# Kernel tuning notes

Hardware: AMD Instinct MI355X
Metric: run time of the kernel (lower is better)

Reference implementation:

```python
import jax, jax.numpy as jnp
import numpy as np

D_MODEL = 256      # cfg.d_model
D_INPUT = 64       # cfg.d_input == n_bands
MEM = 10           # cfg.memory_length
NSYNC = 32         # cfg.n_synch_out
ITERS = 2          # cfg.iterations (internal CTM ticks per audio frame)
VOCAB = 15
MINW = 16          # SynapseUNET minimum width; depth=2 -> widths [256, 16]
MHD = 2            # memory_hidden_dims
SYNC_DIM = NSYNC * (NSYNC + 1) // 2  # 528 upper-tri pairwise products


def _ln(x, g, b, eps=1e-5):
    m = x.mean(-1, keepdims=True)
    v = ((x - m) ** 2).mean(-1, keepdims=True)
    return (x - m) * jax.lax.rsqrt(v + eps) * g + b


def _glu(x):
    a, b = jnp.split(x, 2, axis=-1)
    return a * jax.nn.sigmoid(b)


def setup_inputs() -> dict:
    key = jax.random.key(0)
    ks = iter(jax.random.split(key, 40))
    def rn(shape, fan_in):
        return jax.random.uniform(next(ks), shape, jnp.float32, -1.0, 1.0) / np.sqrt(fan_in)
    B, T = 16, 1500
    z = jnp.zeros
    o = jnp.ones
    return {
        "batch_features": jax.random.normal(next(ks), (B, T, D_INPUT), jnp.float32),
        # learned initial traces
        "start_trace": rn((D_MODEL, MEM), MEM),
        "start_activated_trace": rn((D_MODEL, MEM), MEM),
        # classic-control backbone: Linear(64->64) + ReLU
        "Wb": rn((D_INPUT, D_INPUT), D_INPUT), "bb": z((D_INPUT,)),
        # SynapseUNET depth=2, widths [256,16]; input dim = d_input + d_model = 320
        "Wf": rn((D_INPUT + D_MODEL, 2 * D_MODEL), D_INPUT + D_MODEL), "bf": z((2 * D_MODEL,)),
        "gf": o((D_MODEL,)), "bef": z((D_MODEL,)),
        "Wd": rn((D_MODEL, 2 * MINW), D_MODEL), "bd": z((2 * MINW,)),
        "gd": o((MINW,)), "bed": z((MINW,)),
        "Wu": rn((MINW, 2 * D_MODEL), MINW), "bu": z((2 * D_MODEL,)),
        "gu": o((D_MODEL,)), "beu": z((D_MODEL,)),
        "gs": o((D_MODEL,)), "bes": z((D_MODEL,)),
        # deep neuron-level models (per-neuron MLP over the memory trace)
        "w1": rn((MEM, D_MODEL, 2 * MHD), MEM), "b1": z((1, D_MODEL, 2 * MHD)),
        "w2": rn((MHD, D_MODEL, 2), MHD), "b2": z((1, D_MODEL, 2)),
        # output head Linear(528 -> 15)
        "Wh": rn((SYNC_DIM, VOCAB), SYNC_DIM), "bh": z((VOCAB,)),
    }


def reference(batch_features, start_trace, start_activated_trace, Wb, bb,
              Wf, bf, gf, bef, Wd, bd, gd, bed, Wu, bu, gu, beu, gs, bes,
              w1, b1, w2, b2, Wh, bh):
    B = batch_features.shape[0]
    iu, ju = np.triu_indices(NSYNC)  # static index pattern (528 pairs)

    st0 = jnp.broadcast_to(start_trace, (B, D_MODEL, MEM))
    ast0 = jnp.broadcast_to(start_activated_trace, (B, D_MODEL, MEM))

    def synapses(x):  # (B, 320) -> (B, 256), U-Net with one down/up level
        h0 = _ln(_glu(x @ Wf + bf), gf, bef)        # (B, 256)
        d1 = _ln(_glu(h0 @ Wd + bd), gd, bed)       # (B, 16)
        u0 = _ln(_glu(d1 @ Wu + bu), gu, beu)       # (B, 256)
        return _ln(u0 + h0, gs, bes)                # skip + LN

    def nlm(trace):  # per-neuron MLP over memory: (B, 256, 10) -> (B, 256)
        h = _glu(jnp.einsum('bdm,mdh->bdh', trace, w1) + b1)  # (B, 256, 2)
        h = _glu(jnp.einsum('bdm,mdh->bdh', h, w2) + b2)      # (B, 256, 1)
        return h[..., 0]

    def step(carry, x_t):
        st, ast = carry
        kv = jax.nn.relu(x_t @ Wb + bb)  # backbone features (B, 64)
        act = ast[:, :, -1]
        for _ in range(ITERS):  # internal CTM ticks (fixed, small)
            pre = jnp.concatenate([kv, act], axis=-1)             # (B, 320)
            state = synapses(pre)                                  # (B, 256)
            st = jnp.concatenate([st[:, :, 1:], state[:, :, None]], axis=-1)
            act = nlm(st)                                          # (B, 256)
            ast = jnp.concatenate([ast[:, :, 1:], act[:, :, None]], axis=-1)
        sel = act[:, :NSYNC]  # 'first-last': out-sync uses first n_synch_out neurons
        sync = (sel[:, :, None] * sel[:, None, :])[:, iu, ju]      # (B, 528)
        return (st, ast), sync @ Wh + bh                            # (B, 15)

    _, logits = jax.lax.scan(step, (st0, ast0), jnp.swapaxes(batch_features, 0, 1))
    return jnp.swapaxes(logits, 0, 1)  # (B, T, vocab)
```

## Files before the change

### kernel.cpp

```cpp
#include <hip/hip_runtime.h>
#include <math.h>

#define T_LEN 1500
#define DM 256
#define DI 64
#define MEMN 10
#define SYNCD 528
#define VOC 15

typedef _Float16 f16x2 __attribute__((ext_vector_type(2)));
typedef _Float16 f16x8 __attribute__((ext_vector_type(8)));

#define FDOT2(a, b, c) __builtin_amdgcn_fdot2((a), (b), (c), false)

static __device__ __forceinline__ float dot8(f16x8 w, f16x8 q, float acc) {
  acc = FDOT2(__builtin_shufflevector(w, w, 0, 1), __builtin_shufflevector(q, q, 0, 1), acc);
  acc = FDOT2(__builtin_shufflevector(w, w, 2, 3), __builtin_shufflevector(q, q, 2, 3), acc);
  acc = FDOT2(__builtin_shufflevector(w, w, 4, 5), __builtin_shufflevector(q, q, 4, 5), acc);
  acc = FDOT2(__builtin_shufflevector(w, w, 6, 7), __builtin_shufflevector(q, q, 6, 7), acc);
  return acc;
}
static __device__ __forceinline__ f16x2 pack2(float a, float b) {
  f16x2 r; r.x = (_Float16)a; r.y = (_Float16)b; return r;
}
static __device__ __forceinline__ float sigm(float x) { return 1.0f / (1.0f + __expf(-x)); }

#define DPP_TERM(x, ctrl, rmask) \
  __int_as_float(__builtin_amdgcn_update_dpp(0, __float_as_int(x), (ctrl), (rmask), 0xF, true))
#define DPPADD(x, ctrl, rmask) (x) += DPP_TERM(x, ctrl, rmask)
#define WSUM2(a, b) do { \
  DPPADD(a, 0x111, 0xF); DPPADD(b, 0x111, 0xF); \
  DPPADD(a, 0x112, 0xF); DPPADD(b, 0x112, 0xF); \
  DPPADD(a, 0x114, 0xF); DPPADD(b, 0x114, 0xF); \
  DPPADD(a, 0x118, 0xF); DPPADD(b, 0x118, 0xF); \
  DPPADD(a, 0x142, 0xA); DPPADD(b, 0x142, 0xA); \
  DPPADD(a, 0x143, 0xC); DPPADD(b, 0x143, 0xC); \
} while (0)
static __device__ __forceinline__ float readlane_f(float x, int l) {
  return __int_as_float(__builtin_amdgcn_readlane(__float_as_int(x), l));
}

struct Params {
  const float *x, *st0, *ast0, *Wb, *bb, *Wf, *bf, *gf, *bef,
              *Wd, *bd, *gd, *bed, *Wu, *bu, *gu, *beu, *gs, *bes,
              *w1, *b1, *w2, *b2, *Wh, *bh;
  float* out;
};

struct Smem {
  float4 W1v[MEMN * DM];
  float4 W2v[DM];
  float4 B1v[DM];
  float2 B2v[DM];
  float Bf[2 * DM];
  float Bu[2 * DM];
  float Bd[32];
  float Gf[DM], Bef[DM], Gu[DM], Beu[DM], Gs[DM], Bes[DM];
  float Gd[16], Bed[16];
  float Bh[16];
  float Bb[DI];
  __attribute__((aligned(16))) float St[MEMN * DM];
  __attribute__((aligned(16))) float H0[DM];
  float Act[DM];
  __attribute__((aligned(16))) float D1[16];
  float X2[2][DI];
  __attribute__((aligned(16))) f16x2 Pre2[160];
  float PartD[16 * 33];
  float PartK[512];
  float PartH[240];
  float2 RedAB[8];
  float2 Red2AB[8];
  float Prod[SYNCD];
  float WhL[SYNCD * VOC];
  int Pair[SYNCD];
};

#define FOR20(X) X(0) X(1) X(2) X(3) X(4) X(5) X(6) X(7) X(8) X(9) \
                 X(10) X(11) X(12) X(13) X(14) X(15) X(16) X(17) X(18) X(19)

#define DECLW(i) f16x8 wa##i, wb##i;
#define LOADW(i) { const float* Wc = P.Wf + (size_t)(p160 + (i) * 8) * 512 + ch; \
  f16x8 ta, tb; \
  _Pragma("unroll") for (int e = 0; e < 8; ++e) { \
    ta[e] = (_Float16)Wc[e * 512]; tb[e] = (_Float16)Wc[e * 512 + 256]; } \
  wa##i = ta; wb##i = tb; }
#define DOT0(i) { f16x8 q = pr8[i]; aA0 = dot8(wa##i, q, aA0); aB0 = dot8(wb##i, q, aB0); }
#define DOT1(i) { f16x8 q = pr8[i]; aA1 = dot8(wa##i, q, aA1); aB1 = dot8(wb##i, q, aB1); }
#define DOTSEQ DOT0(0) DOT1(1) DOT0(2) DOT1(3) DOT0(4) DOT1(5) DOT0(6) DOT1(7) DOT0(8) DOT1(9) \
               DOT0(10) DOT1(11) DOT0(12) DOT1(13) DOT0(14) DOT1(15) DOT0(16) DOT1(17) DOT0(18) DOT1(19)

__global__ __launch_bounds__(512) __attribute__((amdgpu_waves_per_eu(2, 2)))
void ctm_kernel(Params P) {
  const int tid = threadIdx.x;
  const int b = blockIdx.x;
  __shared__ Smem sm_s;
  Smem* sm = &sm_s;

  for (int i = tid; i < MEMN * DM; i += 512) sm->W1v[i] = ((const float4*)P.w1)[i];
  if (tid < DM) {
    float2 a = ((const float2*)P.w2)[tid];
    float2 c = ((const float2*)P.w2)[DM + tid];
    float4 w; w.x = a.x; w.y = a.y; w.z = c.x; w.w = c.y;
    sm->W2v[tid] = w;
    sm->B1v[tid] = ((const float4*)P.b1)[tid];
    sm->B2v[tid] = ((const float2*)P.b2)[tid];
    sm->Gf[tid] = P.gf[tid]; sm->Bef[tid] = P.bef[tid];
    sm->Gu[tid] = P.gu[tid]; sm->Beu[tid] = P.beu[tid];
    sm->Gs[tid] = P.gs[tid]; sm->Bes[tid] = P.bes[tid];
  }
  sm->Bf[tid] = P.bf[tid];
  sm->Bu[tid] = P.bu[tid];
  if (tid < 32) sm->Bd[tid] = P.bd[tid];
  if (tid < 16) { sm->Gd[tid] = P.gd[tid]; sm->Bed[tid] = P.bed[tid]; }
  if (tid < VOC) sm->Bh[tid] = P.bh[tid];
  if (tid < DI) sm->Bb[tid] = P.bb[tid];
  for (int i = tid; i < MEMN * DM; i += 512) {
    int m = i >> 8, d = i & 255;
    sm->St[m * DM + d] = P.st0[d * MEMN + m];
  }
  if (tid < DI) sm->X2[0][tid] = P.x[(size_t)b * T_LEN * DI + tid];
  for (int i = tid; i < SYNCD * VOC; i += 512) sm->WhL[i] = P.Wh[i];
  for (int pp = tid; pp < SYNCD; pp += 512) {
    int i = 0, cum = 0;
    while (pp >= cum + (32 - i)) { cum += 32 - i; ++i; }
    sm->Pair[pp] = (i << 8) | (i + (pp - cum));
  }

  const int p = tid & 1;
  const int ch = tid >> 1;
  const int p160 = p * 160;
  FOR20(DECLW)
  FOR20(LOADW)
  const int jD = tid & 31, kcD = tid >> 5;
  float wd[16];
  #pragma unroll
  for (int q = 0; q < 16; ++q) wd[q] = P.Wd[(kcD * 16 + q) * 32 + jD];
  float wua[8], wub[8];
  #pragma unroll
  for (int q = 0; q < 8; ++q) {
    wua[q] = P.Wu[(p * 8 + q) * 512 + ch];
    wub[q] = P.Wu[(p * 8 + q) * 512 + ch + 256];
  }
  const int jK = tid & 63, kcK = tid >> 6;
  float wbr[8];
  #pragma unroll
  for (int q = 0; q < 8; ++q) wbr[q] = P.Wb[(kcK * 8 + q) * 64 + jK];

  __syncthreads();

  {
    float s = 0.f;
    #pragma unroll
    for (int q = 0; q < 8; ++q) s += sm->X2[0][kcK * 8 + q] * wbr[q];
    sm->PartK[kcK * 64 + jK] = s;
    if ((tid & 3) == 0) {
      int e = tid >> 2;
      float a0 = P.ast0[(2 * e) * MEMN + (MEMN - 1)];
      float a1 = P.ast0[(2 * e + 1) * MEMN + (MEMN - 1)];
      sm->Pre2[32 + e] = pack2(a0, a1);
    }
  }
  __syncthreads();
  if (tid >= 256 && tid < 320) {
    int j = tid - 256;
    float kv = sm->Bb[j];
    #pragma unroll
    for (int kc = 0; kc < 8; ++kc) kv += sm->PartK[kc * 64 + j];
    kv = fmaxf(kv, 0.f);
    float kn = DPP_TERM(kv, 0xB1, 0xF);
    if ((j & 1) == 0) sm->Pre2[j >> 1] = pack2(kv, kn);
  }
  __syncthreads();

  int head = 0;
  for (int t = 0; t < T_LEN; ++t) {
    float xr = 0.f;
    if (tid < DI && t + 1 < T_LEN) xr = P.x[((size_t)b * T_LEN + (t + 1)) * DI + tid];

    for (int it = 0; it < 2; ++it) {
      if (it == 1 && tid < DI) sm->X2[(t + 1) & 1][tid] = xr;
      float aA0 = 0.f, aA1 = 0.f, aB0 = 0.f, aB1 = 0.f;
      const f16x8* pr8 = (const f16x8*)(sm->Pre2 + p * 80);
      DOTSEQ
      float av = aA0 + aA1, bv = aB0 + aB1;
      DPPADD(av, 0xB1, 0xF);
      DPPADD(bv, 0xB1, 0xF);
      av += sm->Bf[ch]; bv += sm->Bf[DM + ch];
      float g = av * sigm(bv);
      float s1 = g, s2 = g * g;
      WSUM2(s1, s2);
      if ((tid & 63) == 63) { float2 r; r.x = s1; r.y = s2; sm->RedAB[tid >> 6] = r; }
      __syncthreads();

      float S1 = 0.f, S2 = 0.f;
      #pragma unroll
      for (int w = 0; w < 8; ++w) { float2 r = sm->RedAB[w]; S1 += r.x; S2 += r.y; }
      float mean = S1 * (1.0f / 512.0f);
      float var = S2 * (1.0f / 512.0f) - mean * mean;
      float h0v = (g - mean) * rsqrtf(var + 1e-5f) * sm->Gf[ch] + sm->Bef[ch];
      if (!p) sm->H0[ch] = h0v;
      __syncthreads();

      {
        float s = 0.f;
        #pragma unroll
        for (int qq = 0; qq < 4; ++qq) {
          float4 hv = ((const float4*)sm->H0)[kcD * 4 + qq];
          s += hv.x * wd[qq * 4 + 0] + hv.y * wd[qq * 4 + 1]
             + hv.z * wd[qq * 4 + 2] + hv.w * wd[qq * 4 + 3];
        }
        sm->PartD[kcD * 33 + jD] = s;
      }
      __syncthreads();

      if (tid < 32) {
        int j = tid & 15;
        float s = 0.f;
        #pragma unroll
        for (int kc = 0; kc < 16; ++kc) s += sm->PartD[kc * 33 + (tid >> 4) * 16 + j];
        float oth = __shfl_xor(s, 16);
        float gg = (s + sm->Bd[j]) * sigm(oth + sm->Bd[16 + j]);
        float t1 = gg, t2 = gg * gg;
        DPPADD(t1, 0x111, 0xF); DPPADD(t2, 0x111, 0xF);
        DPPADD(t1, 0x112, 0xF); DPPADD(t2, 0x112, 0xF);
        DPPADD(t1, 0x114, 0xF); DPPADD(t2, 0x114, 0xF);
        DPPADD(t1, 0x118, 0xF); DPPADD(t2, 0x118, 0xF);
        float T1 = readlane_f(t1, 15), T2 = readlane_f(t2, 15);
        float mn = T1 * (1.0f / 16.0f), vr = T2 * (1.0f / 16.0f) - mn * mn;
        float d1 = (gg - mn) * rsqrtf(vr + 1e-5f) * sm->Gd[j] + sm->Bed[j];
        if (tid < 16) sm->D1[j] = d1;
      }
      __syncthreads();

      float gu;
      {
        const float4* d4 = (const float4*)sm->D1;
        float4 dl = d4[p * 2], dh = d4[p * 2 + 1];
        float ua = dl.x * wua[0] + dl.y * wua[1] + dl.z * wua[2] + dl.w * wua[3]
                 + dh.x * wua[4] + dh.y * wua[5] + dh.z * wua[6] + dh.w * wua[7];
        float ub = dl.x * wub[0] + dl.y * wub[1] + dl.z * wub[2] + dl.w * wub[3]
                 + dh.x * wub[4] + dh.y * wub[5] + dh.z * wub[6] + dh.w * wub[7];
        DPPADD(ua, 0xB1, 0xF);
        DPPADD(ub, 0xB1, 0xF);
        ua += sm->Bu[ch]; ub += sm->Bu[DM + ch];
        gu = ua * sigm(ub);
        float t1 = gu, t2 = gu * gu;
        WSUM2(t1, t2);
        if ((tid & 63) == 63) { float2 r; r.x = t1; r.y = t2; sm->RedAB[tid >> 6] = r; }
      }
      __syncthreads();

      float x2v;
      {
        float U1 = 0.f, U2 = 0.f;
        #pragma unroll
        for (int w = 0; w < 8; ++w) { float2 r = sm->RedAB[w]; U1 += r.x; U2 += r.y; }
        float mn = U1 * (1.0f / 512.0f), vr = U2 * (1.0f / 512.0f) - mn * mn;
        float u0 = (gu - mn) * rsqrtf(vr + 1e-5f) * sm->Gu[ch] + sm->Beu[ch];
        x2v = u0 + h0v;
        float t1 = x2v, t2 = x2v * x2v;
        WSUM2(t1, t2);
        if ((tid & 63) == 63) { float2 r; r.x = t1; r.y = t2; sm->Red2AB[tid >> 6] = r; }
      }
      __syncthreads();

      {
        float V1 = 0.f, V2 = 0.f;
        #pragma unroll
        for (int w = 0; w < 8; ++w) { float2 r = sm->Red2AB[w]; V1 += r.x; V2 += r.y; }
        float mn = V1 * (1.0f / 512.0f), vr = V2 * (1.0f / 512.0f) - mn * mn;
        float state = (x2v - mn) * rsqrtf(vr + 1e-5f) * sm->Gs[ch] + sm->Bes[ch];
        if (!p) sm->St[head * DM + ch] = state;
        float4 h1 = sm->B1v[ch];
        int base = head + 1; if (base >= MEMN) base -= MEMN;
        #pragma unroll
        for (int m = 0; m < MEMN - 1; ++m) {
          int slot = base + m; if (slot >= MEMN) slot -= MEMN;
          float tr = sm->St[slot * DM + ch];
          float4 wv = sm->W1v[m * DM + ch];
          h1.x += tr * wv.x; h1.y += tr * wv.y; h1.z += tr * wv.z; h1.w += tr * wv.w;
        }
        {
          float4 wv = sm->W1v[(MEMN - 1) * DM + ch];
          h1.x += state * wv.x; h1.y += state * wv.y; h1.z += state * wv.z; h1.w += state * wv.w;
        }
        float g0 = h1.x * sigm(h1.z), g1 = h1.y * sigm(h1.w);
        float4 w2v = sm->W2v[ch];
        float2 b2v = sm->B2v[ch];
        float o0 = g0 * w2v.x + g1 * w2v.z + b2v.x;
        float o1 = g0 * w2v.y + g1 * w2v.w + b2v.y;
        float act = o0 * sigm(o1);
        if (!p) sm->Act[ch] = act;
        float an = DPP_TERM(act, 0x4E, 0xF);
        if ((tid & 3) == 0) sm->Pre2[32 + (tid >> 2)] = pack2(act, an);
        head += 1; if (head >= MEMN) head = 0;
      }
      __syncthreads();
    }

    {
      int pr = sm->Pair[tid];
      sm->Prod[tid] = sm->Act[pr >> 8] * sm->Act[pr & 255];
      if (tid < SYNCD - 512) {
        int pr2 = sm->Pair[512 + tid];
        sm->Prod[512 + tid] = sm->Act[pr2 >> 8] * sm->Act[pr2 & 255];
      }
      const float* X = sm->X2[(t + 1) & 1];
      float s = 0.f;
      #pragma unroll
      for (int q = 0; q < 8; ++q) s += X[kcK * 8 + q] * wbr[q];
      sm->PartK[kcK * 64 + jK] = s;
      if (t > 0 && tid < VOC) {
        float o = sm->Bh[tid];
        #pragma unroll
        for (int kc2 = 0; kc2 < 16; ++kc2) o += sm->PartH[kc2 * 15 + tid];
        P.out[((size_t)b * T_LEN + (t - 1)) * VOC + tid] = o;
      }
    }
    __syncthreads();

    if (tid < 240) {
      int kc = (tid * 4370) >> 16;
      int v = tid - kc * 15;
      float s = 0.f;
      #pragma unroll
      for (int q = 0; q < 33; ++q) {
        int pp = kc * 33 + q;
        s += sm->Prod[pp] * sm->WhL[pp * 15 + v];
      }
      sm->PartH[kc * 15 + v] = s;
    } else if (tid >= 256 && tid < 320) {
      int j = tid - 256;
      float kv = sm->Bb[j];
      #pragma unroll
      for (int kc = 0; kc < 8; ++kc) kv += sm->PartK[kc * 64 + j];
      kv = fmaxf(kv, 0.f);
      float kn = DPP_TERM(kv, 0xB1, 0xF);
      if ((j & 1) == 0) sm->Pre2[j >> 1] = pack2(kv, kn);
    }
    __syncthreads();
  }

  if (tid < VOC) {
    float o = sm->Bh[tid];
    #pragma unroll
    for (int kc = 0; kc < 16; ++kc) o += sm->PartH[kc * 15 + tid];
    P.out[((size_t)b * T_LEN + (T_LEN - 1)) * VOC + tid] = o;
  }
}

extern "C" void kernel_launch(void* const* d_in, const int* in_sizes, int n_in,
                              void* d_out, int out_size, void* d_ws, size_t ws_size,
                              hipStream_t stream) {
  (void)d_ws; (void)ws_size; (void)n_in; (void)out_size;
  Params P;
  P.x   = (const float*)d_in[0];
  P.st0 = (const float*)d_in[1];
  P.ast0= (const float*)d_in[2];
  P.Wb  = (const float*)d_in[3];
  P.bb  = (const float*)d_in[4];
  P.Wf  = (const float*)d_in[5];
  P.bf  = (const float*)d_in[6];
  P.gf  = (const float*)d_in[7];
  P.bef = (const float*)d_in[8];
  P.Wd  = (const float*)d_in[9];
  P.bd  = (const float*)d_in[10];
  P.gd  = (const float*)d_in[11];
  P.bed = (const float*)d_in[12];
  P.Wu  = (const float*)d_in[13];
  P.bu  = (const float*)d_in[14];
  P.gu  = (const float*)d_in[15];
  P.beu = (const float*)d_in[16];
  P.gs  = (const float*)d_in[17];
  P.bes = (const float*)d_in[18];
  P.w1  = (const float*)d_in[19];
  P.b1  = (const float*)d_in[20];
  P.w2  = (const float*)d_in[21];
  P.b2  = (const float*)d_in[22];
  P.Wh  = (const float*)d_in[23];
  P.bh  = (const float*)d_in[24];
  P.out = (float*)d_out;

  int B = in_sizes[0] / (T_LEN * DI);
  hipLaunchKernelGGL(ctm_kernel, dim3(B), dim3(512), 0, stream, P);
}
```

Baseline: 12.81 ms.

## Fuse two layernorm reductions into one by algebraic expansion of second-norm statistics

The second layernorm's sum and sum-of-squares are expanded algebraically in terms of moments of the GLU output, gamma and the residual term. All nine moments are reduced in one wave/block pass, which removes a full block barrier and reduction round from each of the two internal ticks. The sums of Gu and Gu squared are precomputed once before the time loop. This adds more DPP reduction work per round and may lose precision through cancellation in the expanded variance.

```diff
diff --git a/kernel.cpp b/kernel.cpp
--- a/kernel.cpp
+++ b/kernel.cpp
@@ -35,6 +35,11 @@
   DPPADD(a, 0x118, 0xF); DPPADD(b, 0x118, 0xF); \
   DPPADD(a, 0x142, 0xA); DPPADD(b, 0x142, 0xA); \
   DPPADD(a, 0x143, 0xC); DPPADD(b, 0x143, 0xC); \
+} while (0)
+#define ST9(ctrl, rm) do { \
+  DPPADD(v0, ctrl, rm); DPPADD(v1, ctrl, rm); DPPADD(v2, ctrl, rm); \
+  DPPADD(v3, ctrl, rm); DPPADD(v4, ctrl, rm); DPPADD(v5, ctrl, rm); \
+  DPPADD(v6, ctrl, rm); DPPADD(v7, ctrl, rm); DPPADD(v8, ctrl, rm); \
 } while (0)
 static __device__ __forceinline__ float readlane_f(float x, int l) {
   return __int_as_float(__builtin_amdgcn_readlane(__float_as_int(x), l));
@@ -69,7 +74,8 @@
   float PartK[512];
   float PartH[240];
   float2 RedAB[8];
-  float2 Red2AB[8];
+  __attribute__((aligned(16))) float RedW[8][12];
+  float SGc[4];
   float Prod[SYNCD];
   float WhL[SYNCD * VOC];
   int Pair[SYNCD];
@@ -159,8 +165,18 @@
       float a1 = P.ast0[(2 * e + 1) * MEMN + (MEMN - 1)];
       sm->Pre2[32 + e] = pack2(a0, a1);
     }
+    float gv = sm->Gu[ch];
+    float gv2 = gv * gv;
+    WSUM2(gv, gv2);
+    if ((tid & 63) == 63) { float2 r; r.x = gv; r.y = gv2; sm->RedAB[tid >> 6] = r; }
   }
   __syncthreads();
+  if (tid == 0) {
+    float sg = 0.f, sg2 = 0.f;
+    #pragma unroll
+    for (int w = 0; w < 8; ++w) { float2 r = sm->RedAB[w]; sg += r.x; sg2 += r.y; }
+    sm->SGc[0] = sg; sm->SGc[1] = sg2;
+  }
   if (tid >= 256 && tid < 320) {
     int j = tid - 256;
     float kv = sm->Bb[j];
@@ -232,7 +248,7 @@
       }
       __syncthreads();
 
-      float gu;
+      float gu, Gch, Cch;
       {
         const float4* d4 = (const float4*)sm->D1;
         float4 dl = d4[p * 2], dh = d4[p * 2 + 1];
@@ -244,40 +260,63 @@
         DPPADD(ub, 0xB1, 0xF);
         ua += sm->Bu[ch]; ub += sm->Bu[DM + ch];
         gu = ua * sigm(ub);
-        float t1 = gu, t2 = gu * gu;
-        WSUM2(t1, t2);
-        if ((tid & 63) == 63) { float2 r; r.x = t1; r.y = t2; sm->RedAB[tid >> 6] = r; }
-      }
-      __syncthreads();
-
-      float x2v;
+        Gch = sm->Gu[ch];
+        Cch = sm->Beu[ch] + h0v;
+        float A = gu * Gch;
+        float v0 = gu, v1 = gu * gu, v2 = A, v3 = A * A, v4 = A * Cch,
+              v5 = A * Gch, v6 = Cch, v7 = Cch * Cch, v8 = Gch * Cch;
+        ST9(0x111, 0xF);
+        ST9(0x112, 0xF);
+        ST9(0x114, 0xF);
+        ST9(0x118, 0xF);
+        ST9(0x142, 0xA);
+        ST9(0x143, 0xC);
+        if ((tid & 63) == 63) {
+          float4* rw = (float4*)sm->RedW[tid >> 6];
+          float4 q0; q0.x = v0; q0.y = v1; q0.z = v2; q0.w = v3;
+          float4 q1; q1.x = v4; q1.y = v5; q1.z = v6; q1.w = v7;
+          float4 q2; q2.x = v8; q2.y = 0.f; q2.z = 0.f; q2.w = 0.f;
+          rw[0] = q0; rw[1] = q1; rw[2] = q2;
+        }
+      }
+      __syncthreads();
+
       {
-        float U1 = 0.f, U2 = 0.f;
+        float4 a0; a0.x = 0.f; a0.y = 0.f; a0.z = 0.f; a0.w = 0.f;
+        float4 a1 = a0, a2 = a0;
         #pragma unroll
-        for (int w = 0; w < 8; ++w) { float2 r = sm->RedAB[w]; U1 += r.x; U2 += r.y; }
-        float mn = U1 * (1.0f / 512.0f), vr = U2 * (1.0f / 512.0f) - mn * mn;
-        float u0 = (gu - mn) * rsqrtf(vr + 1e-5f) * sm->Gu[ch] + sm->Beu[ch];
-        x2v = u0 + h0v;
-        float t1 = x2v, t2 = x2v * x2v;
-        WSUM2(t1, t2);
-        if ((tid & 63) == 63) { float2 r; r.x = t1; r.y = t2; sm->Red2AB[tid >> 6] = r; }
-      }
-      __syncthreads();
-
-      {
-        float V1 = 0.f, V2 = 0.f;
-        #pragma unroll
-        for (int w = 0; w < 8; ++w) { float2 r = sm->Red2AB[w]; V1 += r.x; V2 += r.y; }
-        float mn = V1 * (1.0f / 512.0f), vr = V2 * (1.0f / 512.0f) - mn * mn;
-        float state = (x2v - mn) * rsqrtf(vr + 1e-5f) * sm->Gs[ch] + sm->Bes[ch];
+        for (int w = 0; w < 8; ++w) {
+          const float4* rw = (const float4*)sm->RedW[w];
+          float4 q0 = rw[0], q1 = rw[1], q2 = rw[2];
+          a0.x += q0.x; a0.y += q0.y; a0.z += q0.z; a0.w += q0.w;
+          a1.x += q1.x; a1.y += q1.y; a1.z += q1.z; a1.w += q1.w;
+          a2.x += q2.x;
+        }
+        float Sgu = a0.x, Sgu2 = a0.y, SA = a0.z, SA2 = a0.w;
+        float SAC = a1.x, SAG = a1.y, SC = a1.z, SC2 = a1.w;
+        float SGC = a2.x;
+        float SG = sm->SGc[0], SG2 = sm->SGc[1];
+        float m = Sgu * (1.0f / 512.0f);
+        float vr_ = Sgu2 * (1.0f / 512.0f) - m * m;
+        float r = rsqrtf(vr_ + 1e-5f);
+        float u0 = (gu - m) * r * Gch + (Cch - h0v);
+        float x2v = u0 + h0v;
+        float rm = r * m;
+        float S1x = r * SA - rm * SG + SC;
+        float S2x = r * r * SA2 + SC2 + rm * rm * SG2
+                  + 2.0f * r * SAC - 2.0f * r * rm * SAG - 2.0f * rm * SGC;
+        float mx = S1x * (1.0f / 512.0f);
+        float varx = S2x * (1.0f / 512.0f) - mx * mx;
+        float rx = rsqrtf(varx + 1e-5f);
+        float state = (x2v - mx) * rx * sm->Gs[ch] + sm->Bes[ch];
         if (!p) sm->St[head * DM + ch] = state;
         float4 h1 = sm->B1v[ch];
         int base = head + 1; if (base >= MEMN) base -= MEMN;
         #pragma unroll
-        for (int m = 0; m < MEMN - 1; ++m) {
-          int slot = base + m; if (slot >= MEMN) slot -= MEMN;
+        for (int mm = 0; mm < MEMN - 1; ++mm) {
+          int slot = base + mm; if (slot >= MEMN) slot -= MEMN;
           float tr = sm->St[slot * DM + ch];
-          float4 wv = sm->W1v[m * DM + ch];
+          float4 wv = sm->W1v[mm * DM + ch];
           h1.x += tr * wv.x; h1.y += tr * wv.y; h1.z += tr * wv.z; h1.w += tr * wv.w;
         }
         {
```

Result: slower. 18.50 ms (+44.4%).

## Pack two batch elements per 1024-thread block sharing weight tables

Applied to the files above, without the earlier changes.

Each workgroup now processes two batch elements with 1024 threads, sharing the LDS weight tables while giving each element its own private state buffers. With B=16 this halves the grid to 8 blocks. The intent is presumably to cut the redundant per-block weight staging and share one CU's LDS. The cost is that both elements run on one CU and sync at every barrier, and waves_per_eu rises to 4, which halves the per-thread register budget even though each thread still holds 40 f16x8 weight registers, so spilling is likely.

```diff
diff --git a/kernel.cpp b/kernel.cpp
--- a/kernel.cpp
+++ b/kernel.cpp
@@ -47,6 +47,21 @@
   float* out;
 };
 
+struct SmemEl {
+  __attribute__((aligned(16))) float St[MEMN * DM];
+  __attribute__((aligned(16))) float H0[DM];
+  float Act[DM];
+  __attribute__((aligned(16))) float D1[16];
+  float X2[2][DI];
+  __attribute__((aligned(16))) f16x2 Pre2[160];
+  float PartD[16 * 33];
+  float PartK[512];
+  float PartH[240];
+  float2 RedAB[8];
+  float2 Red2AB[8];
+  float Prod[SYNCD];
+};
+
 struct Smem {
   float4 W1v[MEMN * DM];
   float4 W2v[DM];
@@ -59,20 +74,9 @@
   float Gd[16], Bed[16];
   float Bh[16];
   float Bb[DI];
-  __attribute__((aligned(16))) float St[MEMN * DM];
-  __attribute__((aligned(16))) float H0[DM];
-  float Act[DM];
-  __attribute__((aligned(16))) float D1[16];
-  float X2[2][DI];
-  __attribute__((aligned(16))) f16x2 Pre2[160];
-  float PartD[16 * 33];
-  float PartK[512];
-  float PartH[240];
-  float2 RedAB[8];
-  float2 Red2AB[8];
-  float Prod[SYNCD];
   float WhL[SYNCD * VOC];
   int Pair[SYNCD];
+  SmemEl el[2];
 };
 
 #define FOR20(X) X(0) X(1) X(2) X(3) X(4) X(5) X(6) X(7) X(8) X(9) \
@@ -89,14 +93,17 @@
 #define DOTSEQ DOT0(0) DOT1(1) DOT0(2) DOT1(3) DOT0(4) DOT1(5) DOT0(6) DOT1(7) DOT0(8) DOT1(9) \
                DOT0(10) DOT1(11) DOT0(12) DOT1(13) DOT0(14) DOT1(15) DOT0(16) DOT1(17) DOT0(18) DOT1(19)
 
-__global__ __launch_bounds__(512) __attribute__((amdgpu_waves_per_eu(2, 2)))
+__global__ __launch_bounds__(1024) __attribute__((amdgpu_waves_per_eu(4, 4)))
 void ctm_kernel(Params P) {
   const int tid = threadIdx.x;
-  const int b = blockIdx.x;
+  const int elid = tid >> 9;
+  const int ltid = tid & 511;
+  const int b = blockIdx.x * 2 + elid;
   __shared__ Smem sm_s;
   Smem* sm = &sm_s;
-
-  for (int i = tid; i < MEMN * DM; i += 512) sm->W1v[i] = ((const float4*)P.w1)[i];
+  SmemEl* E = &sm_s.el[elid];
+
+  for (int i = tid; i < MEMN * DM; i += 1024) sm->W1v[i] = ((const float4*)P.w1)[i];
   if (tid < DM) {
     float2 a = ((const float2*)P.w2)[tid];
     float2 c = ((const float2*)P.w2)[DM + tid];
@@ -108,30 +115,30 @@
     sm->Gu[tid] = P.gu[tid]; sm->Beu[tid] = P.beu[tid];
     sm->Gs[tid] = P.gs[tid]; sm->Bes[tid] = P.bes[tid];
   }
-  sm->Bf[tid] = P.bf[tid];
-  sm->Bu[tid] = P.bu[tid];
+  if (tid < 2 * DM) { sm->Bf[tid] = P.bf[tid]; sm->Bu[tid] = P.bu[tid]; }
   if (tid < 32) sm->Bd[tid] = P.bd[tid];
   if (tid < 16) { sm->Gd[tid] = P.gd[tid]; sm->Bed[tid] = P.bed[tid]; }
   if (tid < VOC) sm->Bh[tid] = P.bh[tid];
   if (tid < DI) sm->Bb[tid] = P.bb[tid];
-  for (int i = tid; i < MEMN * DM; i += 512) {
-    int m = i >> 8, d = i & 255;
-    sm->St[m * DM + d] = P.st0[d * MEMN + m];
-  }
-  if (tid < DI) sm->X2[0][tid] = P.x[(size_t)b * T_LEN * DI + tid];
-  for (int i = tid; i < SYNCD * VOC; i += 512) sm->WhL[i] = P.Wh[i];
-  for (int pp = tid; pp < SYNCD; pp += 512) {
+  for (int i = tid; i < SYNCD * VOC; i += 1024) sm->WhL[i] = P.Wh[i];
+  for (int pp = tid; pp < SYNCD; pp += 1024) {
     int i = 0, cum = 0;
     while (pp >= cum + (32 - i)) { cum += 32 - i; ++i; }
     sm->Pair[pp] = (i << 8) | (i + (pp - cum));
   }
 
-  const int p = tid & 1;
-  const int ch = tid >> 1;
+  for (int i = ltid; i < MEMN * DM; i += 512) {
+    int m = i >> 8, d = i & 255;
+    E->St[m * DM + d] = P.st0[d * MEMN + m];
+  }
+  if (ltid < DI) E->X2[0][ltid] = P.x[(size_t)b * T_LEN * DI + ltid];
+
+  const int p = ltid & 1;
+  const int ch = ltid >> 1;
   const int p160 = p * 160;
   FOR20(DECLW)
   FOR20(LOADW)
-  const int jD = tid & 31, kcD = tid >> 5;
+  const int jD = ltid & 31, kcD = ltid >> 5;
   float wd[16];
   #pragma unroll
   for (int q = 0; q < 16; ++q) wd[q] = P.Wd[(kcD * 16 + q) * 32 + jD];
@@ -141,7 +148,7 @@
     wua[q] = P.Wu[(p * 8 + q) * 512 + ch];
     wub[q] = P.Wu[(p * 8 + q) * 512 + ch + 256];
   }
-  const int jK = tid & 63, kcK = tid >> 6;
+  const int jK = ltid & 63, kcK = ltid >> 6;
   float wbr[8];
   #pragma unroll
   for (int q = 0; q < 8; ++q) wbr[q] = P.Wb[(kcK * 8 + q) * 64 + jK];
@@ -151,36 +158,36 @@
   {
     float s = 0.f;
     #pragma unroll
-    for (int q = 0; q < 8; ++q) s += sm->X2[0][kcK * 8 + q] * wbr[q];
-    sm->PartK[kcK * 64 + jK] = s;
-    if ((tid & 3) == 0) {
-      int e = tid >> 2;
+    for (int q = 0; q < 8; ++q) s += E->X2[0][kcK * 8 + q] * wbr[q];
+    E->PartK[kcK * 64 + jK] = s;
+    if ((ltid & 3) == 0) {
+      int e = ltid >> 2;
       float a0 = P.ast0[(2 * e) * MEMN + (MEMN - 1)];
       float a1 = P.ast0[(2 * e + 1) * MEMN + (MEMN - 1)];
-      sm->Pre2[32 + e] = pack2(a0, a1);
+      E->Pre2[32 + e] = pack2(a0, a1);
     }
   }
   __syncthreads();
-  if (tid >= 256 && tid < 320) {
-    int j = tid - 256;
+  if (ltid >= 256 && ltid < 320) {
+    int j = ltid - 256;
     float kv = sm->Bb[j];
     #pragma unroll
-    for (int kc = 0; kc < 8; ++kc) kv += sm->PartK[kc * 64 + j];
+    for (int kc = 0; kc < 8; ++kc) kv += E->PartK[kc * 64 + j];
     kv = fmaxf(kv, 0.f);
     float kn = DPP_TERM(kv, 0xB1, 0xF);
-    if ((j & 1) == 0) sm->Pre2[j >> 1] = pack2(kv, kn);
+    if ((j & 1) == 0) E->Pre2[j >> 1] = pack2(kv, kn);
   }
   __syncthreads();
 
   int head = 0;
   for (int t = 0; t < T_LEN; ++t) {
     float xr = 0.f;
-    if (tid < DI && t + 1 < T_LEN) xr = P.x[((size_t)b * T_LEN + (t + 1)) * DI + tid];
+    if (ltid < DI && t + 1 < T_LEN) xr = P.x[((size_t)b * T_LEN + (t + 1)) * DI + ltid];
 
     for (int it = 0; it < 2; ++it) {
-      if (it == 1 && tid < DI) sm->X2[(t + 1) & 1][tid] = xr;
+      if (it == 1 && ltid < DI) E->X2[(t + 1) & 1][ltid] = xr;
       float aA0 = 0.f, aA1 = 0.f, aB0 = 0.f, aB1 = 0.f;
-      const f16x8* pr8 = (const f16x8*)(sm->Pre2 + p * 80);
+      const f16x8* pr8 = (const f16x8*)(E->Pre2 + p * 80);
       DOTSEQ
       float av = aA0 + aA1, bv = aB0 + aB1;
       DPPADD(av, 0xB1, 0xF);
@@ -189,35 +196,35 @@
       float g = av * sigm(bv);
       float s1 = g, s2 = g * g;
       WSUM2(s1, s2);
-      if ((tid & 63) == 63) { float2 r; r.x = s1; r.y = s2; sm->RedAB[tid >> 6] = r; }
+      if ((ltid & 63) == 63) { float2 r; r.x = s1; r.y = s2; E->RedAB[ltid >> 6] = r; }
       __syncthreads();
 
       float S1 = 0.f, S2 = 0.f;
       #pragma unroll
-      for (int w = 0; w < 8; ++w) { float2 r = sm->RedAB[w]; S1 += r.x; S2 += r.y; }
+      for (int w = 0; w < 8; ++w) { float2 r = E->RedAB[w]; S1 += r.x; S2 += r.y; }
       float mean = S1 * (1.0f / 512.0f);
       float var = S2 * (1.0f / 512.0f) - mean * mean;
       float h0v = (g - mean) * rsqrtf(var + 1e-5f) * sm->Gf[ch] + sm->Bef[ch];
-      if (!p) sm->H0[ch] = h0v;
+      if (!p) E->H0[ch] = h0v;
       __syncthreads();
 
       {
         float s = 0.f;
         #pragma unroll
         for (int qq = 0; qq < 4; ++qq) {
-          float4 hv = ((const float4*)sm->H0)[kcD * 4 + qq];
+          float4 hv = ((const float4*)E->H0)[kcD * 4 + qq];
           s += hv.x * wd[qq * 4 + 0] + hv.y * wd[qq * 4 + 1]
              + hv.z * wd[qq * 4 + 2] + hv.w * wd[qq * 4 + 3];
         }
-        sm->PartD[kcD * 33 + jD] = s;
-      }
-      __syncthreads();
-
-      if (tid < 32) {
-        int j = tid & 15;
+        E->PartD[kcD * 33 + jD] = s;
+      }
+      __syncthreads();
+
+      if (ltid < 32) {
+        int j = ltid & 15;
         float s = 0.f;
         #pragma unroll
-        for (int kc = 0; kc < 16; ++kc) s += sm->PartD[kc * 33 + (tid >> 4) * 16 + j];
+        for (int kc = 0; kc < 16; ++kc) s += E->PartD[kc * 33 + (ltid >> 4) * 16 + j];
         float oth = __shfl_xor(s, 16);
         float gg = (s + sm->Bd[j]) * sigm(oth + sm->Bd[16 + j]);
         float t1 = gg, t2 = gg * gg;
@@ -228,13 +235,13 @@
         float T1 = readlane_f(t1, 15), T2 = readlane_f(t2, 15);
         float mn = T1 * (1.0f / 16.0f), vr = T2 * (1.0f / 16.0f) - mn * mn;
         float d1 = (gg - mn) * rsqrtf(vr + 1e-5f) * sm->Gd[j] + sm->Bed[j];
-        if (tid < 16) sm->D1[j] = d1;
+        if (ltid < 16) E->D1[j] = d1;
       }
       __syncthreads();
 
       float gu;
       {
-        const float4* d4 = (const float4*)sm->D1;
+        const float4* d4 = (const float4*)E->D1;
         float4 dl = d4[p * 2], dh = d4[p * 2 + 1];
         float ua = dl.x * wua[0] + dl.y * wua[1] + dl.z * wua[2] + dl.w * wua[3]
                  + dh.x * wua[4] + dh.y * wua[5] + dh.z * wua[6] + dh.w * wua[7];
@@ -246,7 +253,7 @@
         gu = ua * sigm(ub);
         float t1 = gu, t2 = gu * gu;
         WSUM2(t1, t2);
-        if ((tid & 63) == 63) { float2 r; r.x = t1; r.y = t2; sm->RedAB[tid >> 6] = r; }
+        if ((ltid & 63) == 63) { float2 r; r.x = t1; r.y = t2; E->RedAB[ltid >> 6] = r; }
       }
       __syncthreads();
 
@@ -254,29 +261,29 @@
       {
         float U1 = 0.f, U2 = 0.f;
         #pragma unroll
-        for (int w = 0; w < 8; ++w) { float2 r = sm->RedAB[w]; U1 += r.x; U2 += r.y; }
+        for (int w = 0; w < 8; ++w) { float2 r = E->RedAB[w]; U1 += r.x; U2 += r.y; }
         float mn = U1 * (1.0f / 512.0f), vr = U2 * (1.0f / 512.0f) - mn * mn;
         float u0 = (gu - mn) * rsqrtf(vr + 1e-5f) * sm->Gu[ch] + sm->Beu[ch];
         x2v = u0 + h0v;
         float t1 = x2v, t2 = x2v * x2v;
         WSUM2(t1, t2);
-        if ((tid & 63) == 63) { float2 r; r.x = t1; r.y = t2; sm->Red2AB[tid >> 6] = r; }
+        if ((ltid & 63) == 63) { float2 r; r.x = t1; r.y = t2; E->Red2AB[ltid >> 6] = r; }
       }
       __syncthreads();
 
       {
         float V1 = 0.f, V2 = 0.f;
         #pragma unroll
-        for (int w = 0; w < 8; ++w) { float2 r = sm->Red2AB[w]; V1 += r.x; V2 += r.y; }
+        for (int w = 0; w < 8; ++w) { float2 r = E->Red2AB[w]; V1 += r.x; V2 += r.y; }
         float mn = V1 * (1.0f / 512.0f), vr = V2 * (1.0f / 512.0f) - mn * mn;
         float state = (x2v - mn) * rsqrtf(vr + 1e-5f) * sm->Gs[ch] + sm->Bes[ch];
-        if (!p) sm->St[head * DM + ch] = state;
+        if (!p) E->St[head * DM + ch] = state;
         float4 h1 = sm->B1v[ch];
         int base = head + 1; if (base >= MEMN) base -= MEMN;
         #pragma unroll
         for (int m = 0; m < MEMN - 1; ++m) {
           int slot = base + m; if (slot >= MEMN) slot -= MEMN;
-          float tr = sm->St[slot * DM + ch];
+          float tr = E->St[slot * DM + ch];
           float4 wv = sm->W1v[m * DM + ch];
           h1.x += tr * wv.x; h1.y += tr * wv.y; h1.z += tr * wv.z; h1.w += tr * wv.w;
         }
@@ -290,62 +297,62 @@
         float o0 = g0 * w2v.x + g1 * w2v.z + b2v.x;
         float o1 = g0 * w2v.y + g1 * w2v.w + b2v.y;
         float act = o0 * sigm(o1);
-        if (!p) sm->Act[ch] = act;
+        if (!p) E->Act[ch] = act;
         float an = DPP_TERM(act, 0x4E, 0xF);
-        if ((tid & 3) == 0) sm->Pre2[32 + (tid >> 2)] = pack2(act, an);
+        if ((ltid & 3) == 0) E->Pre2[32 + (ltid >> 2)] = pack2(act, an);
         head += 1; if (head >= MEMN) head = 0;
       }
       __syncthreads();
     }
 
     {
-      int pr = sm->Pair[tid];
-      sm->Prod[tid] = sm->Act[pr >> 8] * sm->Act[pr & 255];
-      if (tid < SYNCD - 512) {
-        int pr2 = sm->Pair[512 + tid];
-        sm->Prod[512 + tid] = sm->Act[pr2 >> 8] * sm->Act[pr2 & 255];
-      }
-      const float* X = sm->X2[(t + 1) & 1];
+      int pr = sm->Pair[ltid];
+      E->Prod[ltid] = E->Act[pr >> 8] * E->Act[pr & 255];
+      if (ltid < SYNCD - 512) {
+        int pr2 = sm->Pair[512 + ltid];
+        E->Prod[512 + ltid] = E->Act[pr2 >> 8] * E->Act[pr2 & 255];
+      }
+      const float* X = E->X2[(t + 1) & 1];
       float s = 0.f;
       #pragma unroll
       for (int q = 0; q < 8; ++q) s += X[kcK * 8 + q] * wbr[q];
-      sm->PartK[kcK * 64 + jK] = s;
-      if (t > 0 && tid < VOC) {
-        float o = sm->Bh[tid];
-        #pragma unroll
-        for (int kc2 = 0; kc2 < 16; ++kc2) o += sm->PartH[kc2 * 15 + tid];
-        P.out[((size_t)b * T_LEN + (t - 1)) * VOC + tid] = o;
+      E->PartK[kcK * 64 + jK] = s;
+      if (t > 0 && ltid < VOC) {
+        float o = sm->Bh[ltid];
+        #pragma unroll
+        for (int kc2 = 0; kc2 < 16; ++kc2) o += E->PartH[kc2 * 15 + ltid];
+        P.out[((size_t)b * T_LEN + (t - 1)) * VOC + ltid] = o;
       }
     }
     __syncthreads();
 
-    if (tid < 240) {
-      int kc = (tid * 4370) >> 16;
-      int v = tid - kc * 15;
+    if (ltid < 240) {
+      int kc = (ltid * 4370) >> 16;
+      int v = ltid - kc * 15;
       float s = 0.f;
       #pragma unroll
       for (int q = 0; q < 33; ++q) {
         int pp = kc * 33 + q;
-        s += sm->Prod[pp] * sm->WhL[pp * 15 + v];
-      }
-      sm->PartH[kc * 15 + v] = s;
-    } else if (tid >= 256 && tid < 320) {
-      int j = tid - 256;
+        s += E->Prod[pp] * sm->WhL[pp * 15 + v];
+      }
+      E->PartH[kc * 15 + v] = s;
+    } else if (ltid >= 256 && ltid < 320) {
+      int j = ltid - 256;
       float kv = sm->Bb[j];
       #pragma unroll
-      for (int kc = 0; kc < 8; ++kc) kv += sm->PartK[kc * 64 + j];
+      for (int kc = 0; kc < 8; ++kc) kv += E->PartK[kc * 64 + j];
       kv = fmaxf(kv, 0.f);
       float kn = DPP_TERM(kv, 0xB1, 0xF);
-      if ((j & 1) == 0) sm->Pre2[j >> 1] = pack2(kv, kn);
+      if ((j & 1) == 0) E->Pre2[j >> 1] = pack2(kv, kn);
     }
     __syncthreads();
   }
 
-  if (tid < VOC) {
-    float o = sm->Bh[tid];
+  if (ltid < VOC) {
+    float o = sm->Bh[ltid];
     #pragma unroll
-    for (int kc = 0; kc < 16; ++kc) o += sm->PartH[kc * 15 + tid];
-    P.out[((size_t)b * T_LEN + (T_LEN - 1)) * VOC + tid] = o;
+    for (int kc = 0; kc < 16; ++kc) o += E->PartH[kc * 15 + ltid];
+    P.out[((size_t)b * T_LEN + (T_LEN - 1)) * VOC + ltid] = o;
   }
 }
 
@@ -382,5 +389,5 @@
   P.out = (float*)d_out;
 
   int B = in_sizes[0] / (T_LEN * DI);
-  hipLaunchKernelGGL(ctm_kernel, dim3(B), dim3(512), 0, stream, P);
-}
+  hipLaunchKernelGGL(ctm_kernel, dim3(B / 2), dim3(1024), 0, stream, P);
+}
```

New measurement: 44.37 ms. 3.46x slower.
